# Performance work log

Hardware: AMD Instinct MI355X
Metric: run time of the kernel (lower is better)

Reference implementation:

```python
import jax, jax.numpy as jnp
import numpy as np
from jax import lax

SEQLEN = 99  # hardcoded in the original module


def setup_inputs() -> dict:
    key = jax.random.key(0)
    ks = jax.random.split(key, 9)
    B, L, d = 4096, 100, 256
    q_embed_data = jax.random.normal(ks[0], (B, L, d), dtype=jnp.float32)
    qa_embed_data = jax.random.normal(ks[1], (B, L, d), dtype=jnp.float32)
    # learned params: exp (1,d) xavier-ish, three Linear(2d, d)
    lim = float(np.sqrt(6.0 / (1 + d)))
    exp = jax.random.uniform(ks[2], (1, d), minval=-lim, maxval=lim, dtype=jnp.float32)
    s = 1.0 / np.sqrt(2 * d)
    Wg = jax.random.uniform(ks[3], (d, 2 * d), minval=-s, maxval=s, dtype=jnp.float32)
    bg = jax.random.uniform(ks[4], (d,), minval=-s, maxval=s, dtype=jnp.float32)
    Wk = jax.random.uniform(ks[5], (d, 2 * d), minval=-s, maxval=s, dtype=jnp.float32)
    bk = jax.random.uniform(ks[6], (d,), minval=-s, maxval=s, dtype=jnp.float32)
    Wr = jax.random.uniform(ks[7], (d, 2 * d), minval=-s, maxval=s, dtype=jnp.float32)
    br = jax.random.uniform(ks[8], (d,), minval=-s, maxval=s, dtype=jnp.float32)
    return {"q_embed_data": q_embed_data, "qa_embed_data": qa_embed_data,
            "exp": exp, "Wg": Wg, "bg": bg, "Wk": Wk, "bk": bk, "Wr": Wr, "br": br}


def reference(q_embed_data, qa_embed_data, exp, Wg, bg, Wk, bk, Wr, br):
    B, L, d = qa_embed_data.shape
    # After the 1-step left-pad shift, step i (1..99) consumes qa[:, i-1], q[:, i-1]
    x = jnp.concatenate([qa_embed_data[:, :SEQLEN], q_embed_data[:, :SEQLEN]], axis=-1)  # (B,99,2d)
    # Gates depend only on inputs, not on the recurrent state -> batch the GEMMs
    gate = jax.nn.sigmoid(jnp.einsum('btk,dk->btd', x, Wg) + bg)
    k_q = jnp.tanh(jnp.einsum('btk,dk->btd', x, Wk) + bk)
    reset = jax.nn.sigmoid(jnp.einsum('btk,dk->btd', x, Wr) + br)
    gain = gate * k_q  # (B,99,d)
    exp0 = jnp.broadcast_to(exp, (B, d))

    def step(h, inp):
        r_t, g_t = inp  # each (B,d)
        h_new = r_t * h + (1.0 - r_t) * g_t
        return h_new, h_new

    _, hs = lax.scan(step, exp0, (jnp.swapaxes(reset, 0, 1), jnp.swapaxes(gain, 0, 1)))
    # hs: (99,B,d) -> prepend initial state -> (B,100,d)
    return jnp.concatenate([exp0[:, None, :], jnp.swapaxes(hs, 0, 1)], axis=1)
```

## Files before the change

### kernel.cpp

```cpp
#include <hip/hip_runtime.h>
#include <hip/hip_bf16.h>


typedef __attribute__((ext_vector_type(4))) float f32x4;
typedef __attribute__((ext_vector_type(8))) short short8;

union BF8 { short8 s; unsigned short u[8]; unsigned int w4[4]; };

static constexpr int QROWS    = 100;
static constexpr int QT_BYTES = QROWS * 512;

__device__ __forceinline__ unsigned short f2bf(float f) {
  unsigned int u = __float_as_uint(f);
  return (unsigned short)((u + 0x7fffu + ((u >> 16) & 1u)) >> 16);
}

__device__ __forceinline__ unsigned int pk2bf(float lo, float hi) {
  __hip_bfloat162 h = __float22bfloat162_rn(make_float2(lo, hi));
  union { __hip_bfloat162 h2; unsigned int u; } cv;
  cv.h2 = h;
  return cv.u;
}

__device__ __forceinline__ float sigm(float x) { return 1.f / (1.f + __expf(-x)); }
__device__ __forceinline__ float tanh_(float x) {
  x = fminf(fmaxf(x, -15.f), 15.f);
  float e = __expf(2.f * x);
  return (e - 1.f) / (e + 1.f);
}

__global__ void pack_w(const float* __restrict__ Wg, const float* __restrict__ Wk,
                       const float* __restrict__ Wr, unsigned short* __restrict__ out) {
  int idx = blockIdx.x * 256 + threadIdx.x;
  int l = idx & 63;
  int rest = idx >> 6;
  int ks = rest & 15;
  int nt = rest >> 4;
  int sel = nt >> 4;
  const float* W = (sel == 0) ? Wg : ((sel == 1) ? Wk : Wr);
  int n = ((nt & 15) * 16) + (l & 15);
  const float* p = W + (size_t)n * 512 + ks * 32 + ((l >> 4) * 8);
  unsigned short* o = out + (size_t)idx * 8;
#pragma unroll
  for (int j = 0; j < 8; ++j) o[j] = f2bf(p[j]);
}

template <bool PACKED>
__device__ __forceinline__ short8 ldB(const unsigned short* __restrict__ wpk,
                                      const float* __restrict__ W,
                                      int nt_global, int ks, int l) {
  if constexpr (PACKED) {
    return *(const short8*)(wpk + (((size_t)nt_global * 16 + ks) * 64 + l) * 8);
  } else {
    int n = ((nt_global & 15) * 16) + (l & 15);
    const float* p = W + (size_t)n * 512 + ks * 32 + ((l >> 4) * 8);
    f32x4 v0 = *(const f32x4*)p;
    f32x4 v1 = *(const f32x4*)(p + 4);
    BF8 r;
#pragma unroll
    for (int j = 0; j < 4; ++j) { r.u[j] = f2bf(v0[j]); r.u[4 + j] = f2bf(v1[j]); }
    return r.s;
  }
}

template <bool PACKED>
__global__ __launch_bounds__(512, 1) void fused_kernel(
    const float* __restrict__ q, const float* __restrict__ qa,
    const float* __restrict__ expw,
    const float* __restrict__ Wg, const float* __restrict__ bg,
    const float* __restrict__ Wk, const float* __restrict__ bk,
    const float* __restrict__ Wr, const float* __restrict__ br,
    const unsigned short* __restrict__ wpk,
    float* __restrict__ out) {
  __shared__ char smem[2 * QT_BYTES];
  const int g = blockIdx.x;
  const int dhalf = (g >> 3) & 1;
  const int b = (g & 7) | ((g >> 4) << 3);
  const int tid = threadIdx.x;
  const int w = tid >> 6;
  const int l = tid & 63;
  const int lrow = l & 15;
  const int lgrp = l >> 4;
  const int ntb = dhalf * 8 + w;

  const float* xqa = qa + (size_t)b * 25600;
  const float* xq  = q  + (size_t)b * 25600;

#define DMA_STAGE(qq, bufi)                                                   \
  {                                                                           \
    const float* srcb = ((qq) < 2 ? xqa : xq) + ((qq) & 1) * 128;             \
    for (int w2 = w; w2 < 50; w2 += 8) {                                      \
      int r   = 2 * w2 + (l >> 5);                                            \
      int sl  = l & 31;                                                       \
      int k16 = (sl - 9 * r) & 31;                                            \
      const float* src = srcb + r * 256 + k16 * 4;                            \
      char* dst = smem + (bufi) * QT_BYTES + w2 * 1024;                       \
      __builtin_amdgcn_global_load_lds(                                       \
          (const __attribute__((address_space(1))) unsigned int*)src,         \
          (__attribute__((address_space(3))) unsigned int*)dst, 16, 0, 0);    \
    }                                                                         \
  }

  DMA_STAGE(0, 0);
  DMA_STAGE(1, 1);
  __syncthreads();

  f32x4 accG[7], accK[7], accR[7];
#pragma unroll
  for (int mt = 0; mt < 7; ++mt) {
    accG[mt] = (f32x4){0.f, 0.f, 0.f, 0.f};
    accK[mt] = (f32x4){0.f, 0.f, 0.f, 0.f};
    accR[mt] = (f32x4){0.f, 0.f, 0.f, 0.f};
  }

  int rowOff[7], r9[7];
#pragma unroll
  for (int mt = 0; mt < 7; ++mt) {
    int t = mt * 16 + lrow;
    t = (t > 98) ? 98 : t;
    rowOff[mt] = t * 512;
    r9[mt] = (9 * t) & 31;
  }

#pragma unroll
  for (int qq = 0; qq < 4; ++qq) {
    if (qq == 1) DMA_STAGE(2, 0);
    if (qq == 2) DMA_STAGE(3, 1);
    const char* base = smem + (qq & 1) * QT_BYTES;
#pragma unroll
    for (int kk = 0; kk < 4; ++kk) {
      const int ks = qq * 4 + kk;
      BF8 aF[7];
#pragma unroll
      for (int mt = 0; mt < 7; ++mt) {
        int s0 = (kk * 8 + lgrp * 2 + r9[mt]) & 31;
        int s1 = (s0 + 1) & 31;
        f32x4 v0 = *(const f32x4*)(base + rowOff[mt] + s0 * 16);
        f32x4 v1 = *(const f32x4*)(base + rowOff[mt] + s1 * 16);
        aF[mt].w4[0] = pk2bf(v0[0], v0[1]);
        aF[mt].w4[1] = pk2bf(v0[2], v0[3]);
        aF[mt].w4[2] = pk2bf(v1[0], v1[1]);
        aF[mt].w4[3] = pk2bf(v1[2], v1[3]);
      }
      short8 bG = ldB<PACKED>(wpk, Wg, ntb, ks, l);
#pragma unroll
      for (int mt = 0; mt < 7; ++mt)
        accG[mt] = __builtin_amdgcn_mfma_f32_16x16x32_bf16(aF[mt].s, bG, accG[mt], 0, 0, 0);
      short8 bK = ldB<PACKED>(wpk, Wk, 16 + ntb, ks, l);
#pragma unroll
      for (int mt = 0; mt < 7; ++mt)
        accK[mt] = __builtin_amdgcn_mfma_f32_16x16x32_bf16(aF[mt].s, bK, accK[mt], 0, 0, 0);
      short8 bR = ldB<PACKED>(wpk, Wr, 32 + ntb, ks, l);
#pragma unroll
      for (int mt = 0; mt < 7; ++mt)
        accR[mt] = __builtin_amdgcn_mfma_f32_16x16x32_bf16(aF[mt].s, bR, accR[mt], 0, 0, 0);
    }
    if (qq < 3) __syncthreads();
  }

  float* ob = out + (size_t)b * 25600;
  {
    const int d = dhalf * 128 + w * 16 + lrow;
    const float bgv = bg[d], bkv = bk[d], brv = br[d];
    float h = expw[d];
    if (lgrp == 0) ob[d] = h;
#pragma unroll
    for (int mt = 0; mt < 7; ++mt) {
      float rr[4], cc[4];
#pragma unroll
      for (int r = 0; r < 4; ++r) {
        const int t = mt * 16 + lgrp * 4 + r;
        if (t < 99) {
          float rv = sigm(accR[mt][r] + brv);
          float gv = sigm(accG[mt][r] + bgv);
          float kv = tanh_(accK[mt][r] + bkv);
          rr[r] = rv;
          cc[r] = (1.f - rv) * (gv * kv);
        } else { rr[r] = 1.f; cc[r] = 0.f; }
      }
      const float A  = ((rr[0] * rr[1]) * rr[2]) * rr[3];
      const float Bc = ((cc[0] * rr[1] + cc[1]) * rr[2] + cc[2]) * rr[3] + cc[3];
      float hcur = h, hstart = h;
#pragma unroll
      for (int gg = 0; gg < 4; ++gg) {
        float ag  = __shfl(A,  lrow + (gg << 4), 64);
        float bg_ = __shfl(Bc, lrow + (gg << 4), 64);
        hstart = (lgrp == gg) ? hcur : hstart;
        hcur = __builtin_fmaf(ag, hcur, bg_);
      }
      h = hcur;
      float hh = hstart;
#pragma unroll
      for (int r = 0; r < 4; ++r) {
        const int t = mt * 16 + lgrp * 4 + r;
        hh = __builtin_fmaf(rr[r], hh, cc[r]);
        if (t < 99) ob[(t + 1) * 256 + d] = hh;
      }
    }
  }
#undef DMA_STAGE
}

extern "C" void kernel_launch(void* const* d_in, const int* in_sizes, int n_in,
                              void* d_out, int out_size, void* d_ws, size_t ws_size,
                              hipStream_t stream) {
  const float* q    = (const float*)d_in[0];
  const float* qa   = (const float*)d_in[1];
  const float* expw = (const float*)d_in[2];
  const float* Wg   = (const float*)d_in[3];
  const float* bg   = (const float*)d_in[4];
  const float* Wk   = (const float*)d_in[5];
  const float* bk   = (const float*)d_in[6];
  const float* Wr   = (const float*)d_in[7];
  const float* br   = (const float*)d_in[8];
  float* out = (float*)d_out;

  const bool packed = ws_size >= (size_t)(48 * 16 * 64 * 8 * 2);

  if (packed) {
    unsigned short* wpk = (unsigned short*)d_ws;
    pack_w<<<192, 256, 0, stream>>>(Wg, Wk, Wr, wpk);
    fused_kernel<true><<<8192, 512, 0, stream>>>(q, qa, expw, Wg, bg, Wk, bk, Wr, br, wpk, out);
  } else {
    fused_kernel<false><<<8192, 512, 0, stream>>>(q, qa, expw, Wg, bg, Wk, bk, Wr, br, nullptr, out);
  }
}
```

Measured before the change: 811.6 us.

## Stage inputs as bf16 in swizzled LDS and raise occupancy target

Replaces the async global-to-LDS fp32 DMA staging with register loads that convert the activation tiles to bf16 once and store them into XOR-swizzled LDS. This halves the LDS footprint, so launch bounds now target 4 blocks per CU instead of 1. The inner loop reads A fragments directly as short8 without repeated conversion, and the three weight loads are hoisted before the MFMA loop. The trade-off is synchronous global loads in the prefetch path, which serialize with compute, and tighter register limits from the higher occupancy target.

After: 1.741 ms. 2.14x slower.

```diff
diff --git a/kernel.cpp b/kernel.cpp
--- a/kernel.cpp
+++ b/kernel.cpp
@@ -7,8 +7,7 @@
 
 union BF8 { short8 s; unsigned short u[8]; unsigned int w4[4]; };
 
-static constexpr int QROWS    = 100;
-static constexpr int QT_BYTES = QROWS * 512;
+static constexpr int QT_BYTES = 99 * 256;
 
 __device__ __forceinline__ unsigned short f2bf(float f) {
   unsigned int u = __float_as_uint(f);
@@ -64,7 +63,7 @@
 }
 
 template <bool PACKED>
-__global__ __launch_bounds__(512, 1) void fused_kernel(
+__global__ __launch_bounds__(512, 4) void fused_kernel(
     const float* __restrict__ q, const float* __restrict__ qa,
     const float* __restrict__ expw,
     const float* __restrict__ Wg, const float* __restrict__ bg,
@@ -86,23 +85,25 @@
   const float* xqa = qa + (size_t)b * 25600;
   const float* xq  = q  + (size_t)b * 25600;
 
-#define DMA_STAGE(qq, bufi)                                                   \
-  {                                                                           \
-    const float* srcb = ((qq) < 2 ? xqa : xq) + ((qq) & 1) * 128;             \
-    for (int w2 = w; w2 < 50; w2 += 8) {                                      \
-      int r   = 2 * w2 + (l >> 5);                                            \
-      int sl  = l & 31;                                                       \
-      int k16 = (sl - 9 * r) & 31;                                            \
-      const float* src = srcb + r * 256 + k16 * 4;                            \
-      char* dst = smem + (bufi) * QT_BYTES + w2 * 1024;                       \
-      __builtin_amdgcn_global_load_lds(                                       \
-          (const __attribute__((address_space(1))) unsigned int*)src,         \
-          (__attribute__((address_space(3))) unsigned int*)dst, 16, 0, 0);    \
-    }                                                                         \
-  }
-
-  DMA_STAGE(0, 0);
-  DMA_STAGE(1, 1);
+#define STAGE(qq, bufi)                                                      \
+  {                                                                          \
+    const float* srcb = ((qq) < 2 ? xqa : xq) + ((qq) & 1) * 128;            \
+    char* dst = smem + (bufi) * QT_BYTES;                                    \
+    _Pragma("unroll")                                                        \
+    for (int it = 0; it < 7; ++it) {                                         \
+      int cid = it * 512 + tid;                                              \
+      if (cid < 3168) {                                                      \
+        int row = cid >> 5, c = cid & 31;                                    \
+        f32x4 v = *(const f32x4*)(srcb + row * 256 + c * 4);                 \
+        unsigned long long pkd =                                             \
+            ((unsigned long long)pk2bf(v[2], v[3]) << 32) | pk2bf(v[0], v[1]); \
+        int byte = row * 256 + ((c * 8) ^ ((row & 7) << 4));                 \
+        *(unsigned long long*)(dst + byte) = pkd;                            \
+      }                                                                      \
+    }                                                                        \
+  }
+
+  STAGE(0, 0);
   __syncthreads();
 
   f32x4 accG[7], accK[7], accR[7];
@@ -113,54 +114,39 @@
     accR[mt] = (f32x4){0.f, 0.f, 0.f, 0.f};
   }
 
-  int rowOff[7], r9[7];
+  int pre[7];
 #pragma unroll
   for (int mt = 0; mt < 7; ++mt) {
     int t = mt * 16 + lrow;
     t = (t > 98) ? 98 : t;
-    rowOff[mt] = t * 512;
-    r9[mt] = (9 * t) & 31;
+    pre[mt] = t * 256 + ((lgrp * 16) ^ ((t & 7) << 4));
   }
 
 #pragma unroll
   for (int qq = 0; qq < 4; ++qq) {
-    if (qq == 1) DMA_STAGE(2, 0);
-    if (qq == 2) DMA_STAGE(3, 1);
+    if (qq < 3) STAGE(qq + 1, (qq + 1) & 1);
     const char* base = smem + (qq & 1) * QT_BYTES;
 #pragma unroll
     for (int kk = 0; kk < 4; ++kk) {
       const int ks = qq * 4 + kk;
-      BF8 aF[7];
+      short8 bG = ldB<PACKED>(wpk, Wg, ntb, ks, l);
+      short8 bK = ldB<PACKED>(wpk, Wk, 16 + ntb, ks, l);
+      short8 bR = ldB<PACKED>(wpk, Wr, 32 + ntb, ks, l);
 #pragma unroll
       for (int mt = 0; mt < 7; ++mt) {
-        int s0 = (kk * 8 + lgrp * 2 + r9[mt]) & 31;
-        int s1 = (s0 + 1) & 31;
-        f32x4 v0 = *(const f32x4*)(base + rowOff[mt] + s0 * 16);
-        f32x4 v1 = *(const f32x4*)(base + rowOff[mt] + s1 * 16);
-        aF[mt].w4[0] = pk2bf(v0[0], v0[1]);
-        aF[mt].w4[1] = pk2bf(v0[2], v0[3]);
-        aF[mt].w4[2] = pk2bf(v1[0], v1[1]);
-        aF[mt].w4[3] = pk2bf(v1[2], v1[3]);
-      }
-      short8 bG = ldB<PACKED>(wpk, Wg, ntb, ks, l);
-#pragma unroll
-      for (int mt = 0; mt < 7; ++mt)
-        accG[mt] = __builtin_amdgcn_mfma_f32_16x16x32_bf16(aF[mt].s, bG, accG[mt], 0, 0, 0);
-      short8 bK = ldB<PACKED>(wpk, Wk, 16 + ntb, ks, l);
-#pragma unroll
-      for (int mt = 0; mt < 7; ++mt)
-        accK[mt] = __builtin_amdgcn_mfma_f32_16x16x32_bf16(aF[mt].s, bK, accK[mt], 0, 0, 0);
-      short8 bR = ldB<PACKED>(wpk, Wr, 32 + ntb, ks, l);
-#pragma unroll
-      for (int mt = 0; mt < 7; ++mt)
-        accR[mt] = __builtin_amdgcn_mfma_f32_16x16x32_bf16(aF[mt].s, bR, accR[mt], 0, 0, 0);
+        BF8 a;
+        a.s = *(const short8*)(base + (pre[mt] ^ (kk * 64)));
+        accG[mt] = __builtin_amdgcn_mfma_f32_16x16x32_bf16(a.s, bG, accG[mt], 0, 0, 0);
+        accK[mt] = __builtin_amdgcn_mfma_f32_16x16x32_bf16(a.s, bK, accK[mt], 0, 0, 0);
+        accR[mt] = __builtin_amdgcn_mfma_f32_16x16x32_bf16(a.s, bR, accR[mt], 0, 0, 0);
+      }
     }
     if (qq < 3) __syncthreads();
   }
 
   float* ob = out + (size_t)b * 25600;
   {
-    const int d = dhalf * 128 + w * 16 + lrow;
+    const int d = ntb * 16 + lrow;
     const float bgv = bg[d], bkv = bk[d], brv = br[d];
     float h = expw[d];
     if (lgrp == 0) ob[d] = h;
@@ -198,7 +184,7 @@
       }
     }
   }
-#undef DMA_STAGE
+#undef STAGE
 }
 
 extern "C" void kernel_launch(void* const* d_in, const int* in_sizes, int n_in,
```
